# Optimization experiments

Measured on AMD Instinct MI355X. Metric: run time of the kernel, lower is better.

## Reference

```python
import jax, jax.numpy as jnp
import numpy as np

N, D, L, H = 4, 512, 2048, 8  # batch, feat_dim, seq_len, num_heads


def setup_inputs() -> dict:
    key = jax.random.key(0)
    k1, k2, k3, k4 = jax.random.split(key, 4)
    x = jax.random.normal(k1, (N, D, L), dtype=jnp.float32)
    w_qkv = jax.random.normal(k2, (3 * D, D, 1), dtype=jnp.float32) * 0.02   # 1x1 conv
    w_dw = jax.random.normal(k3, (3 * D, 1, 3), dtype=jnp.float32) * 0.02    # depthwise k=3
    w_proj = jax.random.normal(k4, (D, D, 1), dtype=jnp.float32) * 0.02      # 1x1 conv
    temperature = jnp.ones((1, H, 1, 1), dtype=jnp.float32)
    return {"x": x, "w_qkv": w_qkv, "w_dw": w_dw, "w_proj": w_proj, "temperature": temperature}


def _conv1x1(x, w):
    # x: (n, c_in, l), w: (c_out, c_in, 1)
    return jnp.einsum('oc,ncl->nol', w[:, :, 0], x)


def _l2norm(t, eps=1e-12):
    # matches F.normalize: t / max(||t||_2, eps) along last dim
    n = jnp.sqrt(jnp.sum(t * t, axis=-1, keepdims=True))
    return t / jnp.maximum(n, eps)


def reference(x, w_qkv, w_dw, w_proj, temperature):
    n, d, l = x.shape
    h = temperature.shape[1]
    dh = d // h

    qkv = _conv1x1(x, w_qkv)                               # (n, 3d, l)
    qkv = jax.lax.conv_general_dilated(
        qkv, w_dw, window_strides=(1,), padding=[(1, 1)],
        dimension_numbers=('NCH', 'OIH', 'NCH'),
        feature_group_count=3 * d)                          # depthwise conv, (n, 3d, l)

    q, k, v = jnp.split(qkv, 3, axis=1)                     # each (n, d, l)
    # (n, d, l) -> (n, h, dh, l) -> (n, h, l, dh)
    q = q.reshape(n, h, dh, l).transpose(0, 1, 3, 2)
    k = k.reshape(n, h, dh, l).transpose(0, 1, 3, 2)
    v = v.reshape(n, h, dh, l).transpose(0, 1, 3, 2)

    q = _l2norm(q)
    k = _l2norm(k)

    scores = jnp.einsum('nhqd,nhkd->nhqk', q, k) * temperature  # (n, h, l, l)
    attn = jax.nn.softmax(scores, axis=-1)
    out = jnp.einsum('nhqk,nhkd->nhqd', attn, v)                # (n, h, l, dh)
    out = out.transpose(0, 1, 3, 2).reshape(n, d, l)            # (n, d, l)
    return _conv1x1(out, w_proj)
```

## Files before the change

kernel.cpp:

```cpp
#include <hip/hip_runtime.h>
#include <hip/hip_bf16.h>
#include <hip/hip_fp16.h>
#include <cstdint>
#include <cstddef>

#define N_B 4
#define D_F 512
#define L_S 2048
#define H_N 8
#define DH  64
#define C3  (3*D_F)

typedef __attribute__((ext_vector_type(8)))  short short8;
typedef __attribute__((ext_vector_type(4)))  float f32x4;
typedef __attribute__((ext_vector_type(16))) float f32x16;

#if __has_builtin(__builtin_amdgcn_exp2f)
#define EXP2F(x) __builtin_amdgcn_exp2f(x)
#else
#define EXP2F(x) __expf((x) * 0.6931471805599453f)
#endif

__device__ __forceinline__ unsigned int pk_bf16(float a, float b) {
    __hip_bfloat162 h = __float22bfloat162_rn(float2{a, b});
    union { __hip_bfloat162 h; unsigned int u; } cv;
    cv.h = h;
    return cv.u;
}
__device__ __forceinline__ unsigned short bf16_rn(float f) {
    union { float f; unsigned int u; } c; c.f = f;
    unsigned int r = c.u + 0x7FFF + ((c.u >> 16) & 1);
    return (unsigned short)(r >> 16);
}
__device__ __forceinline__ float bf16_f(unsigned short h) {
    union { unsigned int u; float f; } c; c.u = ((unsigned int)h) << 16;
    return c.f;
}
__device__ __forceinline__ unsigned short f16_bits(float f) {
    union { __half h; unsigned short u; } c;
    c.h = __float2half(f);
    return c.u;
}

__device__ __forceinline__ void gll16(const unsigned short* g, unsigned short* l) {
    __builtin_amdgcn_global_load_lds(
        (const __attribute__((address_space(1))) unsigned int*)g,
        (__attribute__((address_space(3))) unsigned int*)l,
        16, 0, 0);
}

__global__ __launch_bounds__(256) void cvt_w(const float* __restrict__ wq,
                                             unsigned short* __restrict__ wq_h,
                                             int n4q,
                                             const float* __restrict__ wp,
                                             unsigned short* __restrict__ wp_h,
                                             int n4p) {
    int i = blockIdx.x * 256 + threadIdx.x;
    if (i < n4q) {
        float4 v = ((const float4*)wq)[i];
        ushort4 h;
        h.x = bf16_rn(v.x); h.y = bf16_rn(v.y); h.z = bf16_rn(v.z); h.w = bf16_rn(v.w);
        ((ushort4*)wq_h)[i] = h;
    } else if (i < n4q + n4p) {
        int idx = i - n4q;
        float4 v = ((const float4*)wp)[idx];
        ushort4 h;
        h.x = f16_bits(v.x); h.y = f16_bits(v.y); h.z = f16_bits(v.z); h.w = f16_bits(v.w);
        ((ushort4*)wp_h)[idx] = h;
    }
}

__global__ __launch_bounds__(256) void cvt_xT(const float* __restrict__ x,
                                              unsigned short* __restrict__ xT,
                                              int C) {
    __shared__ float tile[64][65];
    const int tid = threadIdx.x;
    const int l0  = blockIdx.x * 64;
    const int c0  = blockIdx.y * 64;
    const int n   = blockIdx.z;

    const float* xn = x + (size_t)n * C * L_S;
#pragma unroll
    for (int r = 0; r < 16; ++r) {
        int c = r * 4 + (tid >> 6);
        int l = tid & 63;
        tile[c][l] = xn[(size_t)(c0 + c) * L_S + l0 + l];
    }
    __syncthreads();

    unsigned short* xn_t = xT + (size_t)n * L_S * C;
#pragma unroll
    for (int r = 0; r < 8; ++r) {
        int l  = r * 8 + (tid >> 5);
        int cp = tid & 31;
        unsigned int pk = pk_bf16(tile[cp * 2][l], tile[cp * 2 + 1][l]);
        *(unsigned int*)&xn_t[(size_t)(l0 + l) * C + c0 + cp * 2] = pk;
    }
}

template<int FP16, int OUT_BF16>
__global__ __launch_bounds__(256) void gemm_mfma3(const unsigned short* __restrict__ Wd,
                                                  const unsigned short* __restrict__ XT,
                                                  void* __restrict__ Y,
                                                  int O, int C) {
    __shared__ unsigned short Wt[4][128 * 8];
    __shared__ unsigned short Xt[4][128 * 8];

    const int tid  = threadIdx.x;
    const int lane = tid & 63;
    const int w    = tid >> 6;
    const int g    = lane >> 4;
    const int c    = lane & 15;
    const int wr   = (w >> 1) * 64;
    const int wc   = (w & 1) * 64;
    const int l0   = blockIdx.x * 128;
    const int o0   = blockIdx.y * 128;
    const int n    = blockIdx.z;

    const unsigned short* XTn = XT + (size_t)n * L_S * C;

    const int rhalf = (w & 1) * 64;
    const int cpA   = w >> 1;
    const int cpB   = 2 + (w >> 1);
    const size_t wrowA = (size_t)(o0 + rhalf + lane) * C;
    const size_t xrowA = (size_t)(l0 + rhalf + lane) * C;

    f32x4 acc[4][4];
#pragma unroll
    for (int mt = 0; mt < 4; ++mt)
#pragma unroll
        for (int nt = 0; nt < 4; ++nt) acc[mt][nt] = (f32x4){0.f, 0.f, 0.f, 0.f};

    for (int c0 = 0; c0 < C; c0 += 32) {
        __syncthreads();
        gll16(Wd  + wrowA + c0 + cpA * 8, &Wt[cpA][rhalf * 8]);
        gll16(Wd  + wrowA + c0 + cpB * 8, &Wt[cpB][rhalf * 8]);
        gll16(XTn + xrowA + c0 + cpA * 8, &Xt[cpA][rhalf * 8]);
        gll16(XTn + xrowA + c0 + cpB * 8, &Xt[cpB][rhalf * 8]);
        __syncthreads();

        short8 a0[4], b0[4];
#pragma unroll
        for (int mt = 0; mt < 4; ++mt) a0[mt] = *(short8*)&Wt[g][(wr + mt * 16 + c) * 8];
#pragma unroll
        for (int nt = 0; nt < 4; ++nt) b0[nt] = *(short8*)&Xt[g][(wc + nt * 16 + c) * 8];

#pragma unroll
        for (int mt = 0; mt < 4; ++mt)
#pragma unroll
            for (int nt = 0; nt < 4; ++nt) {
                if (FP16)
                    acc[mt][nt] = __builtin_amdgcn_mfma_f32_16x16x32_f16(a0[mt], b0[nt], acc[mt][nt], 0, 0, 0);
                else
                    acc[mt][nt] = __builtin_amdgcn_mfma_f32_16x16x32_bf16(a0[mt], b0[nt], acc[mt][nt], 0, 0, 0);
            }
    }

#pragma unroll
    for (int mt = 0; mt < 4; ++mt) {
#pragma unroll
        for (int r = 0; r < 4; ++r) {
            int oo = o0 + wr + mt * 16 + g * 4 + r;
            size_t rowbase = ((size_t)n * O + oo) * L_S;
#pragma unroll
            for (int nt = 0; nt < 4; ++nt) {
                int ll = l0 + wc + nt * 16 + c;
                if (OUT_BF16)
                    ((unsigned short*)Y)[rowbase + ll] = bf16_rn(acc[mt][nt][r]);
                else
                    ((float*)Y)[rowbase + ll] = acc[mt][nt][r];
            }
        }
    }
}

__global__ __launch_bounds__(256) void fused_qk2(const unsigned short* __restrict__ qkv_bf,
                                                 const float* __restrict__ w_dw,
                                                 const float* __restrict__ temp,
                                                 unsigned short* __restrict__ Qb,
                                                 unsigned short* __restrict__ Kb) {
    __shared__ unsigned short rows[64 * 264];
    __shared__ float wsm[192];
    const int tid = threadIdx.x;
    const int l0  = blockIdx.x * 256;
    const int gg  = blockIdx.y;
    const int n   = blockIdx.z;
    const int head = gg & 7;
    const int ch0  = (gg < 8) ? head * 64 : 512 + head * 64;

    if (tid < 192) wsm[tid] = w_dw[ch0 * 3 + tid];

    const unsigned short* base = qkv_bf + ((size_t)n * C3 + ch0) * L_S;
    for (int f = tid; f < 2048; f += 256) {
        int e = f >> 5, s = f & 31;
        *(uint4*)&rows[e * 264 + s * 8] = *(const uint4*)&base[(size_t)e * L_S + l0 + s * 8];
    }
    if (tid < 64) {
        rows[tid * 264 + 256] = (l0 > 0) ? base[(size_t)tid * L_S + l0 - 1] : (unsigned short)0;
    } else if (tid < 128) {
        int e = tid - 64;
        rows[e * 264 + 257] = (l0 + 256 < L_S) ? base[(size_t)e * L_S + l0 + 256] : (unsigned short)0;
    }
    __syncthreads();

    const int lL = tid;
    const int iL = (lL == 0)   ? 256 : lL - 1;
    const int iR = (lL == 255) ? 257 : lL + 1;
    float y[64];
    float s = 0.f;
#pragma unroll
    for (int e = 0; e < 64; ++e) {
        float a = bf16_f(rows[e * 264 + iL]);
        float b = bf16_f(rows[e * 264 + lL]);
        float d = bf16_f(rows[e * 264 + iR]);
        float v = wsm[e * 3 + 0] * a + wsm[e * 3 + 1] * b + wsm[e * 3 + 2] * d;
        y[e] = v;
        s += v * v;
    }
    float sc = 1.0f / fmaxf(sqrtf(s), 1e-12f);
    if (gg < 8) sc *= temp[head] * 1.44269504088896f;

    const int l = l0 + tid;
    unsigned short* dst = ((gg < 8) ? Qb : Kb) + (size_t)(n * H_N + head) * 8 * L_S * 8;
#pragma unroll
    for (int p = 0; p < 8; ++p) {
        uint4 pk = make_uint4(pk_bf16(y[8 * p + 0] * sc, y[8 * p + 1] * sc),
                              pk_bf16(y[8 * p + 2] * sc, y[8 * p + 3] * sc),
                              pk_bf16(y[8 * p + 4] * sc, y[8 * p + 5] * sc),
                              pk_bf16(y[8 * p + 6] * sc, y[8 * p + 7] * sc));
        *(uint4*)&dst[((size_t)p * L_S + l) * 8] = pk;
    }
}

__global__ __launch_bounds__(256) void fused_v2(const unsigned short* __restrict__ qkv_bf,
                                                const float* __restrict__ w_dw,
                                                unsigned short* __restrict__ Vb) {
    const int tid = threadIdx.x;
    const int e   = tid & 63;
    const int jp  = blockIdx.x * 4 + (tid >> 6);
    const int h   = blockIdx.y;
    const int n   = blockIdx.z;
    const int ch  = 1024 + h * 64 + e;
    const unsigned short* row = qkv_bf + ((size_t)n * C3 + ch) * L_S;
    const int k0 = jp * 8;

    uint4 mv = *(const uint4*)&row[k0];
    unsigned int lw = (jp > 0)   ? *(const unsigned int*)&row[k0 - 2] : 0u;
    unsigned int rw = (jp < 255) ? *(const unsigned int*)&row[k0 + 8] : 0u;

    float v[10];
    v[0] = bf16_f((unsigned short)(lw >> 16));
    v[1] = bf16_f((unsigned short)(mv.x & 0xFFFF));
    v[2] = bf16_f((unsigned short)(mv.x >> 16));
    v[3] = bf16_f((unsigned short)(mv.y & 0xFFFF));
    v[4] = bf16_f((unsigned short)(mv.y >> 16));
    v[5] = bf16_f((unsigned short)(mv.z & 0xFFFF));
    v[6] = bf16_f((unsigned short)(mv.z >> 16));
    v[7] = bf16_f((unsigned short)(mv.w & 0xFFFF));
    v[8] = bf16_f((unsigned short)(mv.w >> 16));
    v[9] = bf16_f((unsigned short)(rw & 0xFFFF));

    float w0 = w_dw[ch * 3 + 0], w1 = w_dw[ch * 3 + 1], w2 = w_dw[ch * 3 + 2];
    unsigned int o[4];
#pragma unroll
    for (int i = 0; i < 4; ++i) {
        float y0 = w0 * v[2 * i + 0] + w1 * v[2 * i + 1] + w2 * v[2 * i + 2];
        float y1 = w0 * v[2 * i + 1] + w1 * v[2 * i + 2] + w2 * v[2 * i + 3];
        o[i] = pk_bf16(y0, y1);
    }
    uint4 ov = make_uint4(o[0], o[1], o[2], o[3]);
    *(uint4*)&Vb[(((size_t)(n * H_N + h) * 256 + jp) * 512) + e * 8] = ov;
}

__global__ __launch_bounds__(512, 4) void attn14(const unsigned short* __restrict__ Qb,
                                                 const unsigned short* __restrict__ Kb,
                                                 const unsigned short* __restrict__ Vb,
                                                 const float* __restrict__ temp,
                                                 unsigned short* __restrict__ aoT) {
    __shared__ unsigned short KV[32768];
    __shared__ float smA[128], smB[128];
    float* OtB = (float*)(KV + 16384);
    float* OtA = (float*)KV;

    const int tid  = threadIdx.x;
    const int lane = tid & 63;
    const int w    = tid >> 6;
    const int g2   = w >> 2;
    const int wv   = w & 3;
    const int c32  = lane & 31;
    const int h    = lane >> 5;
    const int q0   = blockIdx.x * 128;
    const int hd   = blockIdx.y;
    const int n    = blockIdx.z;

    const size_t hb = (size_t)(n * H_N + hd);
    const unsigned short* Qh = Qb + hb * 8 * L_S * 8;
    const unsigned short* Kh = Kb + hb * 8 * L_S * 8;
    const unsigned short* Vh = Vb + hb * 256 * 512;
    const float t2    = temp[hd] * 1.44269504088896f;
    const float negm2 = -fabsf(t2);

    unsigned short* myKV = KV + g2 * 16384;
    unsigned short* Qs   = KV + 24576;

    bool dirA;
    {
        auto tp = __builtin_amdgcn_permlane32_swap((int)lane, (int)(lane + 64), false, false);
        unsigned xv = (unsigned)tp[0];
        bool ok = (lane < 32) ? true : (xv == (unsigned)(lane + 32));
        dirA = (__ballot(ok) == 0xFFFFFFFFFFFFFFFFull);
    }

    for (int tk = w; tk < 48; tk += 8) {
        if (tk < 16) {
            int p = tk >> 1, hh = tk & 1;
            gll16(Qh + ((size_t)p * L_S + q0 + hh * 64 + lane) * 8, Qs + p * 1024 + hh * 512);
        } else if (tk < 24) {
            int p = tk - 16;
            gll16(Kh + ((size_t)p * L_S + lane) * 8, KV + p * 512);
        } else if (tk < 32) {
            int p = tk - 24;
            gll16(Vh + ((size_t)p * 512 + lane * 8), KV + 4096 + p * 512);
        } else if (tk < 40) {
            int p = tk - 32;
            gll16(Kh + ((size_t)p * L_S + 64 + lane) * 8, KV + 16384 + p * 512);
        } else {
            int p = tk - 40;
            gll16(Vh + ((size_t)(8 + p) * 512 + lane * 8), KV + 16384 + 4096 + p * 512);
        }
    }
    __syncthreads();

    short8 qa[4];
#pragma unroll
    for (int es = 0; es < 4; ++es)
        qa[es] = *(short8*)&Qs[(es * 2 + h) * 1024 + (wv * 32 + c32) * 8];
    __syncthreads();

    f32x16 acc0, acc1;
#pragma unroll
    for (int i = 0; i < 16; ++i) { acc0[i] = 0.f; acc1[i] = 0.f; }
    float sumP = 0.f;

    for (int it = 0; it < 16; ++it) {
        const int cur = it & 1;
        const unsigned short* B = myKV + cur * 8192;

        if (it < 15) {
            const int kb = ((it + 1) * 2 + g2) * 64;
            unsigned short* D = myKV + (cur ^ 1) * 8192;
            gll16(Kh + ((size_t)wv * L_S + kb + lane) * 8,            D + wv * 512);
            gll16(Kh + ((size_t)(wv + 4) * L_S + kb + lane) * 8,      D + (wv + 4) * 512);
            gll16(Vh + ((size_t)(kb / 8 + wv) * 512 + lane * 8),      D + 4096 + wv * 512);
            gll16(Vh + ((size_t)(kb / 8 + wv + 4) * 512 + lane * 8),  D + 4096 + (wv + 4) * 512);
        }

        f32x16 sf0, sf1;
#pragma unroll
        for (int i = 0; i < 16; ++i) { sf0[i] = 0.f; sf1[i] = 0.f; }
#pragma unroll
        for (int es = 0; es < 4; ++es) {
            short8 ka0 = *(short8*)&B[(es * 2 + h) * 512 + c32 * 8];
            short8 ka1 = *(short8*)&B[(es * 2 + h) * 512 + (32 + c32) * 8];
            sf0 = __builtin_amdgcn_mfma_f32_32x32x16_bf16(ka0, qa[es], sf0, 0, 0, 0);
            sf1 = __builtin_amdgcn_mfma_f32_32x32x16_bf16(ka1, qa[es], sf1, 0, 0, 0);
        }

        short8 pa[4];
        {
            unsigned int W_[16];
#pragma unroll
            for (int G = 0; G < 4; ++G) {
                float p0 = EXP2F(sf0[4*G+0] + negm2);
                float p1 = EXP2F(sf0[4*G+1] + negm2);
                float p2 = EXP2F(sf0[4*G+2] + negm2);
                float p3 = EXP2F(sf0[4*G+3] + negm2);
                sumP += (p0 + p1) + (p2 + p3);
                W_[2*G]   = pk_bf16(p0, p1);
                W_[2*G+1] = pk_bf16(p2, p3);
                float u0 = EXP2F(sf1[4*G+0] + negm2);
                float u1 = EXP2F(sf1[4*G+1] + negm2);
                float u2 = EXP2F(sf1[4*G+2] + negm2);
                float u3 = EXP2F(sf1[4*G+3] + negm2);
                sumP += (u0 + u1) + (u2 + u3);
                W_[8+2*G]   = pk_bf16(u0, u1);
                W_[8+2*G+1] = pk_bf16(u2, u3);
            }
#pragma unroll
            for (int ks = 0; ks < 4; ++ks) {
                unsigned w0 = dirA ? W_[4*ks]   : W_[4*ks+2];
                unsigned w2 = dirA ? W_[4*ks+2] : W_[4*ks];
                unsigned w1 = dirA ? W_[4*ks+1] : W_[4*ks+3];
                unsigned w3 = dirA ? W_[4*ks+3] : W_[4*ks+1];
                auto r02 = __builtin_amdgcn_permlane32_swap((int)w0, (int)w2, false, false);
                auto r13 = __builtin_amdgcn_permlane32_swap((int)w1, (int)w3, false, false);
                unsigned a0 = dirA ? (unsigned)r02[0] : (unsigned)r02[1];
                unsigned a2 = dirA ? (unsigned)r02[1] : (unsigned)r02[0];
                unsigned a1 = dirA ? (unsigned)r13[0] : (unsigned)r13[1];
                unsigned a3 = dirA ? (unsigned)r13[1] : (unsigned)r13[0];
                uint4 pu = make_uint4(a0, a1, a2, a3);
                pa[ks] = *(short8*)&pu;
            }
        }

#pragma unroll
        for (int ks = 0; ks < 4; ++ks) {
            short8 vb0 = *(short8*)&B[4096 + (ks * 2 + h) * 512 + c32 * 8];
            short8 vb1 = *(short8*)&B[4096 + (ks * 2 + h) * 512 + (32 + c32) * 8];
            acc0 = __builtin_amdgcn_mfma_f32_32x32x16_bf16(pa[ks], vb0, acc0, 0, 0, 0);
            acc1 = __builtin_amdgcn_mfma_f32_32x32x16_bf16(pa[ks], vb1, acc1, 0, 0, 0);
        }

        __syncthreads();
    }

    sumP += __shfl_xor(sumP, 32);

    if (g2 == 1) {
        smB[wv * 32 + c32] = sumP;
#pragma unroll
        for (int r = 0; r < 16; ++r) {
            int ql = (r & 3) + 8 * (r >> 2) + 4 * h;
            int qg = wv * 32 + ql;
            OtB[qg * 64 + c32]      = acc0[r];
            OtB[qg * 64 + 32 + c32] = acc1[r];
        }
    } else {
        smA[wv * 32 + c32] = sumP;
    }
    __syncthreads();

    if (g2 == 0) {
#pragma unroll
        for (int r = 0; r < 16; ++r) {
            int ql = (r & 3) + 8 * (r >> 2) + 4 * h;
            int qg = wv * 32 + ql;
            float inv = 1.0f / (smA[qg] + smB[qg]);
            float v0 = (acc0[r] + OtB[qg * 64 + c32])      * inv;
            float v1 = (acc1[r] + OtB[qg * 64 + 32 + c32]) * inv;
            OtA[qg * 64 + (c32 ^ (qg & 31))]        = v0;
            OtA[qg * 64 + ((32 + c32) ^ (qg & 31))] = v1;
        }
    }
    __syncthreads();

    for (int tt = tid; tt < 8192; tt += 512) {
        int qq = tt >> 6, e = tt & 63;
        float v = OtA[qq * 64 + (e ^ (qq & 31))];
        size_t off = ((size_t)n * L_S + q0 + qq) * D_F + hd * 64 + e;
        aoT[off] = f16_bits(v);
    }
}

extern "C" void kernel_launch(void* const* d_in, const int* in_sizes, int n_in,
                              void* d_out, int out_size, void* d_ws, size_t ws_size,
                              hipStream_t stream) {
    const float* x      = (const float*)d_in[0];
    const float* w_qkv  = (const float*)d_in[1];
    const float* w_dw   = (const float*)d_in[2];
    const float* w_proj = (const float*)d_in[3];
    const float* temp   = (const float*)d_in[4];
    float* out = (float*)d_out;

    const size_t WQE = (size_t)C3 * D_F;
    const size_t WPE = (size_t)D_F * D_F;

    char* ws = (char*)d_ws;
    unsigned short* qkv_bf = (unsigned short*)ws;
    unsigned short* Qb     = (unsigned short*)(ws + 25165824);
    unsigned short* Kb     = (unsigned short*)(ws + 33554432);
    unsigned short* Vb     = (unsigned short*)(ws + 41943040);
    unsigned short* xT     = (unsigned short*)(ws + 50331648);
    unsigned short* wq_h   = (unsigned short*)(ws + 58720256);
    unsigned short* wp_h   = (unsigned short*)(ws + 60293120);
    unsigned short* aoT    = xT;

    cvt_xT<<<dim3(L_S / 64, D_F / 64, N_B), 256, 0, stream>>>(x, xT, D_F);
    {
        int n4q = (int)(WQE / 4), n4p = (int)(WPE / 4);
        cvt_w<<<dim3((n4q + n4p + 255) / 256), 256, 0, stream>>>(
            w_qkv, wq_h, n4q, w_proj, wp_h, n4p);
    }

    gemm_mfma3<0, 1><<<dim3(L_S / 128, C3 / 128, N_B), 256, 0, stream>>>(
        wq_h, xT, qkv_bf, C3, D_F);

    fused_qk2<<<dim3(L_S / 256, 16, N_B), 256, 0, stream>>>(qkv_bf, w_dw, temp, Qb, Kb);
    fused_v2<<<dim3(64, H_N, N_B), 256, 0, stream>>>(qkv_bf, w_dw, Vb);

    attn14<<<dim3(L_S / 128, H_N, N_B), 512, 0, stream>>>(Qb, Kb, Vb, temp, aoT);

    gemm_mfma3<1, 0><<<dim3(L_S / 128, D_F / 128, N_B), 256, 0, stream>>>(
        wp_h, aoT, out, D_F, D_F);
}
```

Baseline: 134.4 us.

## Drop K/V double buffering and shrink LDS to raise attention occupancy

The attention kernel now uses a single K/V LDS buffer per half-group, with barriers before and after each tile load, in place of prefetching the next tile into a second buffer. LDS use is halved and the launch bound asks for 8 blocks per CU. Q fragments are read straight from global memory instead of being staged through LDS, and the epilogue reuses the one buffer. The fixed softmax shift based on temperature is removed. The aim is more resident waves to hide latency, at the cost of losing load/compute overlap, adding extra barriers, and tighter register limits that could cause spills. Without the shift, exp2 could also overflow if temperature is large.

```diff
diff --git a/kernel.cpp b/kernel.cpp
--- a/kernel.cpp
+++ b/kernel.cpp
@@ -272,15 +272,13 @@
     *(uint4*)&Vb[(((size_t)(n * H_N + h) * 256 + jp) * 512) + e * 8] = ov;
 }
 
-__global__ __launch_bounds__(512, 4) void attn14(const unsigned short* __restrict__ Qb,
+__global__ __launch_bounds__(512, 8) void attn15(const unsigned short* __restrict__ Qb,
                                                  const unsigned short* __restrict__ Kb,
                                                  const unsigned short* __restrict__ Vb,
-                                                 const float* __restrict__ temp,
                                                  unsigned short* __restrict__ aoT) {
-    __shared__ unsigned short KV[32768];
+    __shared__ unsigned short KV[16384];
     __shared__ float smA[128], smB[128];
-    float* OtB = (float*)(KV + 16384);
-    float* OtA = (float*)KV;
+    float* OtB = (float*)KV;
 
     const int tid  = threadIdx.x;
     const int lane = tid & 63;
@@ -297,11 +295,6 @@
     const unsigned short* Qh = Qb + hb * 8 * L_S * 8;
     const unsigned short* Kh = Kb + hb * 8 * L_S * 8;
     const unsigned short* Vh = Vb + hb * 256 * 512;
-    const float t2    = temp[hd] * 1.44269504088896f;
-    const float negm2 = -fabsf(t2);
-
-    unsigned short* myKV = KV + g2 * 16384;
-    unsigned short* Qs   = KV + 24576;
 
     bool dirA;
     {
@@ -311,31 +304,12 @@
         dirA = (__ballot(ok) == 0xFFFFFFFFFFFFFFFFull);
     }
 
-    for (int tk = w; tk < 48; tk += 8) {
-        if (tk < 16) {
-            int p = tk >> 1, hh = tk & 1;
-            gll16(Qh + ((size_t)p * L_S + q0 + hh * 64 + lane) * 8, Qs + p * 1024 + hh * 512);
-        } else if (tk < 24) {
-            int p = tk - 16;
-            gll16(Kh + ((size_t)p * L_S + lane) * 8, KV + p * 512);
-        } else if (tk < 32) {
-            int p = tk - 24;
-            gll16(Vh + ((size_t)p * 512 + lane * 8), KV + 4096 + p * 512);
-        } else if (tk < 40) {
-            int p = tk - 32;
-            gll16(Kh + ((size_t)p * L_S + 64 + lane) * 8, KV + 16384 + p * 512);
-        } else {
-            int p = tk - 40;
-            gll16(Vh + ((size_t)(8 + p) * 512 + lane * 8), KV + 16384 + 4096 + p * 512);
-        }
-    }
-    __syncthreads();
-
     short8 qa[4];
 #pragma unroll
     for (int es = 0; es < 4; ++es)
-        qa[es] = *(short8*)&Qs[(es * 2 + h) * 1024 + (wv * 32 + c32) * 8];
-    __syncthreads();
+        qa[es] = *(const short8*)&Qh[((size_t)(es * 2 + h) * L_S + q0 + wv * 32 + c32) * 8];
+
+    unsigned short* myKV = KV + g2 * 8192;
 
     f32x16 acc0, acc1;
 #pragma unroll
@@ -343,17 +317,16 @@
     float sumP = 0.f;
 
     for (int it = 0; it < 16; ++it) {
-        const int cur = it & 1;
-        const unsigned short* B = myKV + cur * 8192;
-
-        if (it < 15) {
-            const int kb = ((it + 1) * 2 + g2) * 64;
-            unsigned short* D = myKV + (cur ^ 1) * 8192;
-            gll16(Kh + ((size_t)wv * L_S + kb + lane) * 8,            D + wv * 512);
-            gll16(Kh + ((size_t)(wv + 4) * L_S + kb + lane) * 8,      D + (wv + 4) * 512);
-            gll16(Vh + ((size_t)(kb / 8 + wv) * 512 + lane * 8),      D + 4096 + wv * 512);
-            gll16(Vh + ((size_t)(kb / 8 + wv + 4) * 512 + lane * 8),  D + 4096 + (wv + 4) * 512);
-        }
+        const int kb = (it * 2 + g2) * 64;
+
+        __syncthreads();
+        gll16(Kh + ((size_t)wv * L_S + kb + lane) * 8,            myKV + wv * 512);
+        gll16(Kh + ((size_t)(wv + 4) * L_S + kb + lane) * 8,      myKV + (wv + 4) * 512);
+        gll16(Vh + ((size_t)(kb / 8 + wv) * 512 + lane * 8),      myKV + 4096 + wv * 512);
+        gll16(Vh + ((size_t)(kb / 8 + wv + 4) * 512 + lane * 8),  myKV + 4096 + (wv + 4) * 512);
+        __syncthreads();
+
+        const unsigned short* B = myKV;
 
         f32x16 sf0, sf1;
 #pragma unroll
@@ -371,17 +344,17 @@
             unsigned int W_[16];
 #pragma unroll
             for (int G = 0; G < 4; ++G) {
-                float p0 = EXP2F(sf0[4*G+0] + negm2);
-                float p1 = EXP2F(sf0[4*G+1] + negm2);
-                float p2 = EXP2F(sf0[4*G+2] + negm2);
-                float p3 = EXP2F(sf0[4*G+3] + negm2);
+                float p0 = EXP2F(sf0[4*G+0]);
+                float p1 = EXP2F(sf0[4*G+1]);
+                float p2 = EXP2F(sf0[4*G+2]);
+                float p3 = EXP2F(sf0[4*G+3]);
                 sumP += (p0 + p1) + (p2 + p3);
                 W_[2*G]   = pk_bf16(p0, p1);
                 W_[2*G+1] = pk_bf16(p2, p3);
-                float u0 = EXP2F(sf1[4*G+0] + negm2);
-                float u1 = EXP2F(sf1[4*G+1] + negm2);
-                float u2 = EXP2F(sf1[4*G+2] + negm2);
-                float u3 = EXP2F(sf1[4*G+3] + negm2);
+                float u0 = EXP2F(sf1[4*G+0]);
+                float u1 = EXP2F(sf1[4*G+1]);
+                float u2 = EXP2F(sf1[4*G+2]);
+                float u3 = EXP2F(sf1[4*G+3]);
                 sumP += (u0 + u1) + (u2 + u3);
                 W_[8+2*G]   = pk_bf16(u0, u1);
                 W_[8+2*G+1] = pk_bf16(u2, u3);
@@ -410,9 +383,8 @@
             acc0 = __builtin_amdgcn_mfma_f32_32x32x16_bf16(pa[ks], vb0, acc0, 0, 0, 0);
             acc1 = __builtin_amdgcn_mfma_f32_32x32x16_bf16(pa[ks], vb1, acc1, 0, 0, 0);
         }
-
-        __syncthreads();
-    }
+    }
+    __syncthreads();
 
     sumP += __shfl_xor(sumP, 32);
 
@@ -431,22 +403,28 @@
     __syncthreads();
 
     if (g2 == 0) {
+        float b0[16], b1[16], inv[16];
 #pragma unroll
         for (int r = 0; r < 16; ++r) {
             int ql = (r & 3) + 8 * (r >> 2) + 4 * h;
             int qg = wv * 32 + ql;
-            float inv = 1.0f / (smA[qg] + smB[qg]);
-            float v0 = (acc0[r] + OtB[qg * 64 + c32])      * inv;
-            float v1 = (acc1[r] + OtB[qg * 64 + 32 + c32]) * inv;
-            OtA[qg * 64 + (c32 ^ (qg & 31))]        = v0;
-            OtA[qg * 64 + ((32 + c32) ^ (qg & 31))] = v1;
+            b0[r] = OtB[qg * 64 + c32];
+            b1[r] = OtB[qg * 64 + 32 + c32];
+            inv[r] = 1.0f / (smA[qg] + smB[qg]);
+        }
+#pragma unroll
+        for (int r = 0; r < 16; ++r) {
+            int ql = (r & 3) + 8 * (r >> 2) + 4 * h;
+            int qg = wv * 32 + ql;
+            OtB[qg * 64 + (c32 ^ (qg & 31))]        = (acc0[r] + b0[r]) * inv[r];
+            OtB[qg * 64 + ((32 + c32) ^ (qg & 31))] = (acc1[r] + b1[r]) * inv[r];
         }
     }
     __syncthreads();
 
     for (int tt = tid; tt < 8192; tt += 512) {
         int qq = tt >> 6, e = tt & 63;
-        float v = OtA[qq * 64 + (e ^ (qq & 31))];
+        float v = OtB[qq * 64 + (e ^ (qq & 31))];
         size_t off = ((size_t)n * L_S + q0 + qq) * D_F + hd * 64 + e;
         aoT[off] = f16_bits(v);
     }
@@ -488,7 +466,7 @@
     fused_qk2<<<dim3(L_S / 256, 16, N_B), 256, 0, stream>>>(qkv_bf, w_dw, temp, Qb, Kb);
     fused_v2<<<dim3(64, H_N, N_B), 256, 0, stream>>>(qkv_bf, w_dw, Vb);
 
-    attn14<<<dim3(L_S / 128, H_N, N_B), 512, 0, stream>>>(Qb, Kb, Vb, temp, aoT);
+    attn15<<<dim3(L_S / 128, H_N, N_B), 512, 0, stream>>>(Qb, Kb, Vb, aoT);
 
     gemm_mfma3<1, 0><<<dim3(L_S / 128, D_F / 128, N_B), 256, 0, stream>>>(
         wp_h, aoT, out, D_F, D_F);
```

Result: slower. 264.4 us (+96.8%).
